# Kernel tuning notes

Hardware: AMD Instinct MI355X
Metric: run time of the kernel (lower is better)

The kernel has to match this reference:

```python
import jax, jax.numpy as jnp
import numpy as np


def setup_inputs() -> dict:
    key = jax.random.key(0)
    ks = jax.random.split(key, 9)
    B, T, D, U = 512, 1024, 64, 128
    inp = {
        'inputs': jax.random.normal(ks[0], (B, T, D), dtype=jnp.float32),
        'W_f': jax.random.normal(ks[1], (D, U), dtype=jnp.float32) * 0.05,
        'U_f': jax.random.normal(ks[2], (U, U), dtype=jnp.float32) * 0.05,
        'b_f': jnp.zeros((U,), dtype=jnp.float32),
        'W_i': jax.random.normal(ks[3], (D, U), dtype=jnp.float32) * 0.05,
        'U_i': jax.random.normal(ks[4], (U, U), dtype=jnp.float32) * 0.05,
        'b_i': jnp.zeros((U,), dtype=jnp.float32),
        'W_c': jax.random.normal(ks[5], (D, U), dtype=jnp.float32) * 0.05,
        'U_c': jax.random.normal(ks[6], (U, U), dtype=jnp.float32) * 0.05,
        'b_c': jnp.zeros((U,), dtype=jnp.float32),
        'W_o': jax.random.normal(ks[7], (D, U), dtype=jnp.float32) * 0.05,
        'U_o': jax.random.normal(ks[8], (U, U), dtype=jnp.float32) * 0.05,
        'b_o': jnp.zeros((U,), dtype=jnp.float32),
    }
    return inp


def _lstm(inputs, W_f, U_f, b_f, W_i, U_i, b_i, W_c, U_c, b_c, W_o, U_o, b_o):
    B, T, D = inputs.shape
    U = W_f.shape[1]
    # Precompute all input-to-gate projections in one batched GEMM per gate: [B,T,U]
    xf = jnp.einsum('btd,du->btu', inputs, W_f) + b_f
    xi = jnp.einsum('btd,du->btu', inputs, W_i) + b_i
    xc = jnp.einsum('btd,du->btu', inputs, W_c) + b_c
    xo = jnp.einsum('btd,du->btu', inputs, W_o) + b_o
    # time-major stacked gate inputs: [T, B, 4, U]
    xg = jnp.stack([xf, xi, xc, xo], axis=2).transpose(1, 0, 2, 3)
    # concatenated recurrent weights: [U, 4U]
    U_all = jnp.concatenate([U_f, U_i, U_c, U_o], axis=1)

    def step(carry, x_t):
        h, c = carry
        # x_t: [B, 4, U]
        rec = (h @ U_all).reshape(B, 4, U)
        g = x_t + rec
        f = jax.nn.sigmoid(g[:, 0])
        i = jax.nn.sigmoid(g[:, 1])
        c_tilde = jnp.tanh(g[:, 2])
        o = jax.nn.sigmoid(g[:, 3])
        c_new = f * c + i * c_tilde
        h_new = o * jnp.tanh(c_new)
        return (h_new, c_new), None

    h0 = jnp.zeros((B, U), dtype=inputs.dtype)
    c0 = jnp.zeros((B, U), dtype=inputs.dtype)
    (h, c), _ = jax.lax.scan(step, (h0, c0), xg)
    return h


def reference(inputs, W_f, U_f, b_f, W_i, U_i, b_i, W_c, U_c, b_c, W_o, U_o, b_o):
    return _lstm(inputs, W_f, U_f, b_f, W_i, U_i, b_i, W_c, U_c, b_c, W_o, U_o, b_o)
```

## Files before the change

kernel.cpp:

```cpp
#include <hip/hip_runtime.h>
#include <stdint.h>


typedef __attribute__((ext_vector_type(8))) short short8;
typedef __attribute__((ext_vector_type(4))) float floatx4;
typedef __attribute__((ext_vector_type(4))) int   intx4;
typedef __attribute__((ext_vector_type(8))) int   intx8;

#define B_SZ   512
#define T_SZ   1024
#define D_SZ   64
#define U_SZ   128
#define ROWS   2
#define NBLK   (B_SZ / ROWS)
#define NTHR   512
#define A1STRB 160
#define GXSTR  524
#define L2E    1.4426950408889634f

__device__ __forceinline__ short f2bf(float f) {
    uint32_t u = __builtin_bit_cast(uint32_t, f);
    uint32_t r = (u + 0x7fffu + ((u >> 16) & 1u)) >> 16;
    return (short)r;
}
__device__ __forceinline__ int cvt2bf(float lo, float hi) {
    int r;
    asm("v_cvt_pk_bf16_f32 %0, %1, %2" : "=v"(r) : "v"(lo), "v"(hi));
    return r;
}
__device__ __forceinline__ short8 pk8(float4 a, float4 b) {
    intx4 t = {cvt2bf(a.x, a.y), cvt2bf(a.z, a.w), cvt2bf(b.x, b.y), cvt2bf(b.z, b.w)};
    return __builtin_bit_cast(short8, t);
}
__device__ __forceinline__ float fsig2(float e) {
    return __builtin_amdgcn_rcpf(1.0f + __builtin_amdgcn_exp2f(e));
}
__device__ __forceinline__ float fth2(float e) {
    return 1.0f - 2.0f * __builtin_amdgcn_rcpf(1.0f + __builtin_amdgcn_exp2f(e));
}
__device__ __forceinline__ float ftanh(float x) {
    return 1.0f - 2.0f * __builtin_amdgcn_rcpf(1.0f + __builtin_amdgcn_exp2f(2.0f * L2E * x));
}
__device__ __forceinline__ void sync_lds() {
    asm volatile("s_waitcnt lgkmcnt(0)\n\ts_barrier" ::: "memory");
}

__global__ __launch_bounds__(NTHR, 2) void lstm_persistent(
    const float* __restrict__ xin,
    const float* __restrict__ Wf, const float* __restrict__ Uf, const float* __restrict__ bfp,
    const float* __restrict__ Wi, const float* __restrict__ Ui, const float* __restrict__ bip,
    const float* __restrict__ Wc, const float* __restrict__ Uc, const float* __restrict__ bcp,
    const float* __restrict__ Wo, const float* __restrict__ Uo, const float* __restrict__ bop,
    float* __restrict__ out)
{
    __shared__ float Gx[2][16 * GXSTR];
    __shared__ __align__(8) char A1[2][2 * A1STRB];

    const int tid  = threadIdx.x;
    const int wave = tid >> 6;
    const int lane = tid & 63;
    const int quad = lane >> 4;
    const int nlo  = lane & 15;
    const int blk  = blockIdx.x;

    const float* Wg[4] = {Wf, Wi, Wc, Wo};
    const float* Ug[4] = {Uf, Ui, Uc, Uo};
    const float* Bg[4] = {bfp, bip, bcp, bop};
    const float scg[4] = {-L2E, -L2E, 2.0f * L2E, -L2E};

    if (wave < 4) {
        __builtin_amdgcn_s_setprio(1);
        const int ti_s = quad & 1;
        const int prow = quad >> 1;
        const int u_s  = 32 * wave + 16 * ti_s + nlo;

        intx8 bU8[4][2];
#pragma unroll
        for (int g = 0; g < 4; ++g)
#pragma unroll
            for (int ti = 0; ti < 2; ++ti) {
                const int uc = 32 * wave + 16 * ti + nlo;
#pragma unroll
                for (int d = 0; d < 8; ++d) {
                    const int k0 = quad * 32 + d * 4;
                    int pk = __builtin_amdgcn_cvt_pk_fp8_f32(
                        Ug[g][(k0 + 0) * U_SZ + uc], Ug[g][(k0 + 1) * U_SZ + uc], 0, 0);
                    pk = __builtin_amdgcn_cvt_pk_fp8_f32(
                        Ug[g][(k0 + 2) * U_SZ + uc], Ug[g][(k0 + 3) * U_SZ + uc], pk, 1);
                    bU8[g][ti][d] = pk;
                }
            }
        float c_st = 0.0f;

        for (int i = tid; i < 2 * 2 * A1STRB; i += 256) ((char*)A1)[i] = 0;
        __syncthreads();

        for (int g = 0; g < 128; ++g) {
            const float* GxR = &Gx[g & 1][0];
#pragma unroll
            for (int j = 0; j < 8; ++j) {
                const char* ap = &A1[j & 1][(nlo >> 3) * A1STRB + quad * 32];
                intx4 alo = *(const intx4*)(ap);
                intx4 ahi = *(const intx4*)(ap + 16);
                floatx4 gx = *(const floatx4*)&GxR[(2 * j + prow) * GXSTR + 4 * u_s];
                intx8 a8 = {alo.x, alo.y, alo.z, alo.w, ahi.x, ahi.y, ahi.z, ahi.w};
                const floatx4 z = (floatx4){0.f, 0.f, 0.f, 0.f};

                floatx4 a00 = __builtin_amdgcn_mfma_scale_f32_16x16x128_f8f6f4(
                    a8, bU8[0][0], z, 0, 0, 0, 0x7f7f7f7f, 0, 0x7f7f7f7f);
                floatx4 a01 = __builtin_amdgcn_mfma_scale_f32_16x16x128_f8f6f4(
                    a8, bU8[0][1], z, 0, 0, 0, 0x7f7f7f7f, 0, 0x7f7f7f7f);
                float fg = fsig2(__builtin_fmaf(ti_s ? a01[0] : a00[0], -L2E, gx[0]));
                floatx4 a10 = __builtin_amdgcn_mfma_scale_f32_16x16x128_f8f6f4(
                    a8, bU8[1][0], z, 0, 0, 0, 0x7f7f7f7f, 0, 0x7f7f7f7f);
                floatx4 a11 = __builtin_amdgcn_mfma_scale_f32_16x16x128_f8f6f4(
                    a8, bU8[1][1], z, 0, 0, 0, 0x7f7f7f7f, 0, 0x7f7f7f7f);
                float ig = fsig2(__builtin_fmaf(ti_s ? a11[0] : a10[0], -L2E, gx[1]));
                floatx4 a20 = __builtin_amdgcn_mfma_scale_f32_16x16x128_f8f6f4(
                    a8, bU8[2][0], z, 0, 0, 0, 0x7f7f7f7f, 0, 0x7f7f7f7f);
                floatx4 a21 = __builtin_amdgcn_mfma_scale_f32_16x16x128_f8f6f4(
                    a8, bU8[2][1], z, 0, 0, 0, 0x7f7f7f7f, 0, 0x7f7f7f7f);
                float ct = fth2(__builtin_fmaf(ti_s ? a21[0] : a20[0], 2.0f * L2E, gx[2]));
                floatx4 a30 = __builtin_amdgcn_mfma_scale_f32_16x16x128_f8f6f4(
                    a8, bU8[3][0], z, 0, 0, 0, 0x7f7f7f7f, 0, 0x7f7f7f7f);
                floatx4 a31 = __builtin_amdgcn_mfma_scale_f32_16x16x128_f8f6f4(
                    a8, bU8[3][1], z, 0, 0, 0, 0x7f7f7f7f, 0, 0x7f7f7f7f);
                float og = fsig2(__builtin_fmaf(ti_s ? a31[0] : a30[0], -L2E, gx[3]));

                float c = fg * c_st + ig * ct;
                float h = og * ftanh(c);
                c_st = c;

                if (g == 127 && j == 7) {
                    out[(size_t)(blk * ROWS + prow) * U_SZ + u_s] = h;
                } else {
                    int pk = __builtin_amdgcn_cvt_pk_fp8_f32(h, h, 0, 0);
                    A1[(j & 1) ^ 1][prow * A1STRB + u_s] = (char)(pk & 0xff);
                }
                sync_lds();
            }
        }
    } else {
        const int p = wave - 4;
        const int brow  = nlo & 1;
        const int t_off = nlo >> 1;

        short8 bWp[8][2];
        float  bw[8];
#pragma unroll
        for (int tau = 0; tau < 8; ++tau) {
            const int gt = tau >> 1;
            const int uc = 16 * (2 * p + (tau & 1)) + nlo;
            bw[tau] = Bg[gt][uc];
#pragma unroll
            for (int kt = 0; kt < 2; ++kt)
#pragma unroll
                for (int jj = 0; jj < 8; ++jj) {
                    int k = kt * 32 + quad * 8 + jj;
                    bWp[tau][kt][jj] = f2bf(Wg[gt][k * U_SZ + uc]);
                }
        }

        const float* xg = xin + ((size_t)(blk * ROWS + brow) * T_SZ) * D_SZ + quad * 8;

        float4 p0 = *(const float4*)(xg + (size_t)t_off * D_SZ + 0);
        float4 p1 = *(const float4*)(xg + (size_t)t_off * D_SZ + 4);
        float4 p2 = *(const float4*)(xg + (size_t)t_off * D_SZ + 32);
        float4 p3 = *(const float4*)(xg + (size_t)t_off * D_SZ + 36);
        float4 q0 = *(const float4*)(xg + (size_t)(8 + t_off) * D_SZ + 0);
        float4 q1 = *(const float4*)(xg + (size_t)(8 + t_off) * D_SZ + 4);
        float4 q2 = *(const float4*)(xg + (size_t)(8 + t_off) * D_SZ + 32);
        float4 q3 = *(const float4*)(xg + (size_t)(8 + t_off) * D_SZ + 36);

        short8 xa0 = pk8(p0, p1);
        short8 xa1 = pk8(p2, p3);
#pragma unroll
        for (int tau = 0; tau < 8; ++tau) {
            const int gt = tau >> 1;
            const int uc = 16 * (2 * p + (tau & 1)) + nlo;
            floatx4 acc = (floatx4){0.f, 0.f, 0.f, 0.f};
            acc = __builtin_amdgcn_mfma_f32_16x16x32_bf16(xa0, bWp[tau][0], acc, 0, 0, 0);
            acc = __builtin_amdgcn_mfma_f32_16x16x32_bf16(xa1, bWp[tau][1], acc, 0, 0, 0);
#pragma unroll
            for (int r = 0; r < 4; ++r)
                Gx[0][(quad * 4 + r) * GXSTR + 4 * uc + gt] = (acc[r] + bw[tau]) * scg[gt];
        }
        xa0 = pk8(q0, q1);
        xa1 = pk8(q2, q3);
        float4 xq0 = *(const float4*)(xg + (size_t)(16 + t_off) * D_SZ + 0);
        float4 xq1 = *(const float4*)(xg + (size_t)(16 + t_off) * D_SZ + 4);
        float4 xq2 = *(const float4*)(xg + (size_t)(16 + t_off) * D_SZ + 32);
        float4 xq3 = *(const float4*)(xg + (size_t)(16 + t_off) * D_SZ + 36);
        __syncthreads();

        short8 xn0 = xa0, xn1 = xa1;
        for (int g = 0; g < 128; ++g) {
            float* GxW = &Gx[(g + 1) & 1][0];
#pragma unroll
            for (int j = 0; j < 8; ++j) {
                if (j == 0 && g <= 125) {
                    xn0 = pk8(xq0, xq1);
                    xn1 = pk8(xq2, xq3);
                }
                if (j == 2 && g <= 124) {
                    const float* b = xg + (size_t)(8 * (g + 3) + t_off) * D_SZ;
                    xq0 = *(const float4*)(b + 0);
                    xq1 = *(const float4*)(b + 4);
                    xq2 = *(const float4*)(b + 32);
                    xq3 = *(const float4*)(b + 36);
                }
                if (g < 127) {
                    const int gt = j >> 1;
                    const int uc = 16 * (2 * p + (j & 1)) + nlo;
                    floatx4 acc = (floatx4){0.f, 0.f, 0.f, 0.f};
                    acc = __builtin_amdgcn_mfma_f32_16x16x32_bf16(xa0, bWp[j][0], acc, 0, 0, 0);
                    acc = __builtin_amdgcn_mfma_f32_16x16x32_bf16(xa1, bWp[j][1], acc, 0, 0, 0);
#pragma unroll
                    for (int r = 0; r < 4; ++r)
                        GxW[(quad * 4 + r) * GXSTR + 4 * uc + gt] = (acc[r] + bw[j]) * scg[gt];
                }
                sync_lds();
            }
            xa0 = xn0; xa1 = xn1;
        }
    }
}

extern "C" void kernel_launch(void* const* d_in, const int* in_sizes, int n_in,
                              void* d_out, int out_size, void* d_ws, size_t ws_size,
                              hipStream_t stream) {
    (void)in_sizes; (void)n_in; (void)d_ws; (void)ws_size; (void)out_size;
    const float* xin = (const float*)d_in[0];
    const float* Wf  = (const float*)d_in[1];
    const float* Uf  = (const float*)d_in[2];
    const float* bf  = (const float*)d_in[3];
    const float* Wi  = (const float*)d_in[4];
    const float* Ui  = (const float*)d_in[5];
    const float* bi  = (const float*)d_in[6];
    const float* Wc  = (const float*)d_in[7];
    const float* Uc  = (const float*)d_in[8];
    const float* bc  = (const float*)d_in[9];
    const float* Wo  = (const float*)d_in[10];
    const float* Uo  = (const float*)d_in[11];
    const float* bo  = (const float*)d_in[12];
    float* out = (float*)d_out;

    hipLaunchKernelGGL(lstm_persistent, dim3(NBLK), dim3(NTHR), 0, stream,
                       xin, Wf, Uf, bf, Wi, Ui, bi, Wc, Uc, bc, Wo, Uo, bo, out);
}
```

Baseline: 617.9 us.

## Process one batch row per block and batch the gate MFMAs

Result: slower. 959.7 us (+55.3%).

```diff
diff --git a/kernel.cpp b/kernel.cpp
--- a/kernel.cpp
+++ b/kernel.cpp
@@ -11,7 +11,7 @@
 #define T_SZ   1024
 #define D_SZ   64
 #define U_SZ   128
-#define ROWS   2
+#define ROWS   1
 #define NBLK   (B_SZ / ROWS)
 #define NTHR   512
 #define A1STRB 160
@@ -106,33 +106,27 @@
                 intx8 a8 = {alo.x, alo.y, alo.z, alo.w, ahi.x, ahi.y, ahi.z, ahi.w};
                 const floatx4 z = (floatx4){0.f, 0.f, 0.f, 0.f};
 
-                floatx4 a00 = __builtin_amdgcn_mfma_scale_f32_16x16x128_f8f6f4(
-                    a8, bU8[0][0], z, 0, 0, 0, 0x7f7f7f7f, 0, 0x7f7f7f7f);
-                floatx4 a01 = __builtin_amdgcn_mfma_scale_f32_16x16x128_f8f6f4(
-                    a8, bU8[0][1], z, 0, 0, 0, 0x7f7f7f7f, 0, 0x7f7f7f7f);
-                float fg = fsig2(__builtin_fmaf(ti_s ? a01[0] : a00[0], -L2E, gx[0]));
-                floatx4 a10 = __builtin_amdgcn_mfma_scale_f32_16x16x128_f8f6f4(
-                    a8, bU8[1][0], z, 0, 0, 0, 0x7f7f7f7f, 0, 0x7f7f7f7f);
-                floatx4 a11 = __builtin_amdgcn_mfma_scale_f32_16x16x128_f8f6f4(
-                    a8, bU8[1][1], z, 0, 0, 0, 0x7f7f7f7f, 0, 0x7f7f7f7f);
-                float ig = fsig2(__builtin_fmaf(ti_s ? a11[0] : a10[0], -L2E, gx[1]));
-                floatx4 a20 = __builtin_amdgcn_mfma_scale_f32_16x16x128_f8f6f4(
-                    a8, bU8[2][0], z, 0, 0, 0, 0x7f7f7f7f, 0, 0x7f7f7f7f);
-                floatx4 a21 = __builtin_amdgcn_mfma_scale_f32_16x16x128_f8f6f4(
-                    a8, bU8[2][1], z, 0, 0, 0, 0x7f7f7f7f, 0, 0x7f7f7f7f);
-                float ct = fth2(__builtin_fmaf(ti_s ? a21[0] : a20[0], 2.0f * L2E, gx[2]));
-                floatx4 a30 = __builtin_amdgcn_mfma_scale_f32_16x16x128_f8f6f4(
-                    a8, bU8[3][0], z, 0, 0, 0, 0x7f7f7f7f, 0, 0x7f7f7f7f);
-                floatx4 a31 = __builtin_amdgcn_mfma_scale_f32_16x16x128_f8f6f4(
-                    a8, bU8[3][1], z, 0, 0, 0, 0x7f7f7f7f, 0, 0x7f7f7f7f);
-                float og = fsig2(__builtin_fmaf(ti_s ? a31[0] : a30[0], -L2E, gx[3]));
+                floatx4 acc0[4], acc1[4];
+#pragma unroll
+                for (int gt = 0; gt < 4; ++gt)
+                    acc0[gt] = __builtin_amdgcn_mfma_scale_f32_16x16x128_f8f6f4(
+                        a8, bU8[gt][0], z, 0, 0, 0, 0x7f7f7f7f, 0, 0x7f7f7f7f);
+#pragma unroll
+                for (int gt = 0; gt < 4; ++gt)
+                    acc1[gt] = __builtin_amdgcn_mfma_scale_f32_16x16x128_f8f6f4(
+                        a8, bU8[gt][1], z, 0, 0, 0, 0x7f7f7f7f, 0, 0x7f7f7f7f);
+
+                float fg = fsig2(__builtin_fmaf(ti_s ? acc1[0][0] : acc0[0][0], -L2E, gx[0]));
+                float ig = fsig2(__builtin_fmaf(ti_s ? acc1[1][0] : acc0[1][0], -L2E, gx[1]));
+                float ct = fth2(__builtin_fmaf(ti_s ? acc1[2][0] : acc0[2][0], 2.0f * L2E, gx[2]));
+                float og = fsig2(__builtin_fmaf(ti_s ? acc1[3][0] : acc0[3][0], -L2E, gx[3]));
 
                 float c = fg * c_st + ig * ct;
                 float h = og * ftanh(c);
                 c_st = c;
 
                 if (g == 127 && j == 7) {
-                    out[(size_t)(blk * ROWS + prow) * U_SZ + u_s] = h;
+                    if (prow == 0) out[(size_t)blk * U_SZ + u_s] = h;
                 } else {
                     int pk = __builtin_amdgcn_cvt_pk_fp8_f32(h, h, 0, 0);
                     A1[(j & 1) ^ 1][prow * A1STRB + u_s] = (char)(pk & 0xff);
@@ -142,7 +136,6 @@
         }
     } else {
         const int p = wave - 4;
-        const int brow  = nlo & 1;
         const int t_off = nlo >> 1;
 
         short8 bWp[8][2];
@@ -161,7 +154,7 @@
                 }
         }
 
-        const float* xg = xin + ((size_t)(blk * ROWS + brow) * T_SZ) * D_SZ + quad * 8;
+        const float* xg = xin + ((size_t)blk * T_SZ) * D_SZ + quad * 8;
 
         float4 p0 = *(const float4*)(xg + (size_t)t_off * D_SZ + 0);
         float4 p1 = *(const float4*)(xg + (size_t)t_off * D_SZ + 4);
```
